# Kernel tuning notes

Measured on AMD Instinct MI355X. Metric: run time of the kernel, lower is better.

Reference implementation:

```python
import jax, jax.numpy as jnp
import numpy as np

N, E = 50000, 800000
C_IN, C_HID, C_OUT = 64, 128, 64
BN_EPS = 1e-5


def setup_inputs() -> dict:
    key = jax.random.key(0)
    ks = jax.random.split(key, 8)
    s1 = 1.0 / np.sqrt(C_IN)
    s2 = 1.0 / np.sqrt(C_HID)
    return {
        "x": jax.random.normal(ks[0], (N, C_IN), dtype=jnp.float32),
        "edge_index": jax.random.randint(ks[1], (2, E), 0, N, dtype=jnp.int64),
        # message MLP: in -> hidden -> out
        "W1": jax.random.uniform(ks[2], (C_IN, C_HID), jnp.float32, -s1, s1),
        "b1": jnp.zeros((C_HID,), jnp.float32),
        "W2": jax.random.uniform(ks[3], (C_HID, C_OUT), jnp.float32, -s2, s2),
        "b2": jnp.zeros((C_OUT,), jnp.float32),
        # root/self transform
        "W_root": jax.random.uniform(ks[4], (C_IN, C_OUT), jnp.float32, -s1, s1),
        "b_root": jnp.zeros((C_OUT,), jnp.float32),
        # PReLU (single shared parameter, torch default 0.25)
        "prelu_w": jnp.full((1,), 0.25, jnp.float32),
        # BatchNorm affine params
        "bn_gamma": jnp.ones((C_OUT,), jnp.float32),
        "bn_beta": jnp.zeros((C_OUT,), jnp.float32),
    }


def reference(x, edge_index, W1, b1, W2, b2, W_root, b_root, prelu_w, bn_gamma, bn_beta):
    src, dst = edge_index[0], edge_index[1]
    # gather -> per-edge message MLP: [E, C_hid] -> [E, C_out]
    m = jax.nn.relu(x[src] @ W1 + b1) @ W2 + b2
    # scatter-sum to destination nodes: [N, C_out]
    agg = jax.ops.segment_sum(m, dst, num_segments=N)
    h = agg + x @ W_root + b_root
    # PReLU
    h = jnp.where(h >= 0, h, prelu_w * h)
    # BatchNorm over nodes (training-mode batch stats, biased var)
    mu = jnp.mean(h, axis=0)
    var = jnp.mean(jnp.square(h - mu), axis=0)
    h = (h - mu) * jax.lax.rsqrt(var + BN_EPS) * bn_gamma + bn_beta
    return h
```

## Files before the change

### kernel.cpp

```cpp
#include <hip/hip_runtime.h>

#define NNODES 50000
#define NEDGES 800000
#define NTILES 3125
#define CAP    64

typedef __attribute__((ext_vector_type(8))) short bf16x8;
typedef __attribute__((ext_vector_type(4))) float f32x4;

union FragU { uint u[4]; bf16x8 v; };

__device__ __forceinline__ uint bfr(float f) {
    uint u = __float_as_uint(f);
    return (u + 0x7fffu + ((u >> 16) & 1u)) >> 16;
}
__device__ __forceinline__ uint pack_bf2(float a, float b) {
    return bfr(a) | (bfr(b) << 16);
}
__device__ __forceinline__ float bf2f(uint hi16) {
    return __uint_as_float(hi16 << 16);
}

__global__ __launch_bounds__(256) void mlp_root_kernel(
    const float* __restrict__ x,
    const float* __restrict__ W1, const float* __restrict__ b1,
    const float* __restrict__ W2, const float* __restrict__ b2,
    const float* __restrict__ Wr, const float* __restrict__ br,
    ushort* __restrict__ M16, float* __restrict__ R)
{
    __shared__ uint  sFrag[40 * 256];
    __shared__ float sb1[128];
    __shared__ float sb2[64];
    __shared__ float sbr[64];
    __shared__ uint  sH[4 * 16 * 68];

    const int tid = threadIdx.x;
    for (int idx = tid; idx < 40 * 256; idx += 256) {
        const int f  = idx >> 8;
        const int ln = (idx >> 2) & 63;
        const int d  = idx & 3;
        const int g = ln >> 4, r = ln & 15;
        const int j0 = 2 * d;
        float w0, w1v;
        if (f < 16) {
            const int mt = f >> 1, ks = f & 1;
            const int k = 32 * ks + 8 * g + j0, c = 16 * mt + r;
            w0 = W1[k * 128 + c];  w1v = W1[(k + 1) * 128 + c];
        } else if (f < 32) {
            const int mt = (f - 16) >> 2, ks = (f - 16) & 3;
            const int k = 32 * ks + 8 * g + j0, c = 16 * mt + r;
            w0 = W2[k * 64 + c];   w1v = W2[(k + 1) * 64 + c];
        } else {
            const int mt = (f - 32) >> 1, ks = (f - 32) & 1;
            const int k = 32 * ks + 8 * g + j0, c = 16 * mt + r;
            w0 = Wr[k * 64 + c];   w1v = Wr[(k + 1) * 64 + c];
        }
        sFrag[idx] = pack_bf2(w0, w1v);
    }
    if (tid < 128) sb1[tid] = b1[tid];
    if (tid < 64)  { sb2[tid] = b2[tid]; sbr[tid] = br[tid]; }
    __syncthreads();

    const int lane = tid & 63;
    const int g = lane >> 4, r = lane & 15;
    uint* Hw = &sH[(tid >> 6) * 16 * 68];
    uint* Mu = (uint*)M16;
    const int gw  = blockIdx.x * 4 + (tid >> 6);
    const int nwv = gridDim.x * 4;

#define LOADFRAG(f) (*(const bf16x8*)&sFrag[((f) << 8) | (lane << 2)])

    for (int t = gw; t < NTILES; t += nwv) {
        const int node = t * 16 + r;
        bf16x8 xf[2];
#pragma unroll
        for (int ks = 0; ks < 2; ++ks) {
            const float4 f0 = *(const float4*)&x[node * 64 + 32 * ks + 8 * g];
            const float4 f1 = *(const float4*)&x[node * 64 + 32 * ks + 8 * g + 4];
            FragU fx;
            fx.u[0] = pack_bf2(f0.x, f0.y); fx.u[1] = pack_bf2(f0.z, f0.w);
            fx.u[2] = pack_bf2(f1.x, f1.y); fx.u[3] = pack_bf2(f1.z, f1.w);
            xf[ks] = fx.v;
        }
#pragma unroll
        for (int mt = 0; mt < 8; ++mt) {
            f32x4 a = {0.f, 0.f, 0.f, 0.f};
            a = __builtin_amdgcn_mfma_f32_16x16x32_bf16(LOADFRAG(2 * mt), xf[0], a, 0, 0, 0);
            a = __builtin_amdgcn_mfma_f32_16x16x32_bf16(LOADFRAG(2 * mt + 1), xf[1], a, 0, 0, 0);
            const int hc = 16 * mt + 4 * g;
            const float v0 = fmaxf(a[0] + sb1[hc + 0], 0.f);
            const float v1 = fmaxf(a[1] + sb1[hc + 1], 0.f);
            const float v2 = fmaxf(a[2] + sb1[hc + 2], 0.f);
            const float v3 = fmaxf(a[3] + sb1[hc + 3], 0.f);
            const int hd = r * 68 + 8 * mt + 2 * g;
            Hw[hd]     = pack_bf2(v0, v1);
            Hw[hd + 1] = pack_bf2(v2, v3);
        }
        bf16x8 hf[4];
#pragma unroll
        for (int ks = 0; ks < 4; ++ks)
            hf[ks] = *(const bf16x8*)&Hw[r * 68 + 16 * ks + 4 * g];
#pragma unroll
        for (int mt = 0; mt < 4; ++mt) {
            f32x4 a2 = {0.f, 0.f, 0.f, 0.f};
#pragma unroll
            for (int ks = 0; ks < 4; ++ks)
                a2 = __builtin_amdgcn_mfma_f32_16x16x32_bf16(LOADFRAG(16 + 4 * mt + ks), hf[ks], a2, 0, 0, 0);
            f32x4 ar = {0.f, 0.f, 0.f, 0.f};
            ar = __builtin_amdgcn_mfma_f32_16x16x32_bf16(LOADFRAG(32 + 2 * mt), xf[0], ar, 0, 0, 0);
            ar = __builtin_amdgcn_mfma_f32_16x16x32_bf16(LOADFRAG(32 + 2 * mt + 1), xf[1], ar, 0, 0, 0);
            const int oc = 16 * mt + 4 * g;
            const float m0 = a2[0] + sb2[oc + 0], m1 = a2[1] + sb2[oc + 1];
            const float m2 = a2[2] + sb2[oc + 2], m3 = a2[3] + sb2[oc + 3];
            uint2 mp = make_uint2(pack_bf2(m0, m1), pack_bf2(m2, m3));
            *(uint2*)&Mu[node * 32 + 8 * mt + 2 * g] = mp;
            float4 rv = make_float4(ar[0] + sbr[oc + 0], ar[1] + sbr[oc + 1],
                                    ar[2] + sbr[oc + 2], ar[3] + sbr[oc + 3]);
            *(float4*)&R[node * 64 + oc] = rv;
        }
    }
#undef LOADFRAG
}

__global__ __launch_bounds__(256) void fill_kernel(
    const int* __restrict__ ei, int* __restrict__ cnt, int* __restrict__ bucket)
{
    const int e = blockIdx.x * 256 + threadIdx.x;
    const int dst = ei[NEDGES + e];
    const int pos = atomicAdd(&cnt[dst], 1);
    if (pos < CAP) bucket[dst * CAP + pos] = ei[e];
}

__global__ __launch_bounds__(256) void gather_prelu_stats_kernel(
    const int* __restrict__ cnt, const int* __restrict__ bucket,
    const ushort* __restrict__ M16, const float* __restrict__ pw,
    float* __restrict__ h, float* __restrict__ stats)
{
    __shared__ float ls[128];
    const int tid = threadIdx.x;
    if (tid < 128) ls[tid] = 0.f;
    __syncthreads();

    const int lane = tid & 63;
    const int gw   = (blockIdx.x * 256 + tid) >> 6;
    const int nwv  = (gridDim.x * 256) >> 6;
    const float p  = pw[0];
    float sum = 0.f, sumsq = 0.f;

    for (int n = gw; n < NNODES; n += nwv) {
        int c = cnt[n]; c = c > CAP ? CAP : c;
        const int sall = bucket[n * CAP + lane];
        float a0 = 0.f, a1 = 0.f, a2 = 0.f, a3 = 0.f;
        int i = 0;
        for (; i + 4 <= c; i += 4) {
            const int s0 = __shfl(sall, i),     s1 = __shfl(sall, i + 1);
            const int s2 = __shfl(sall, i + 2), s3 = __shfl(sall, i + 3);
            a0 += bf2f(M16[s0 * 64 + lane]);
            a1 += bf2f(M16[s1 * 64 + lane]);
            a2 += bf2f(M16[s2 * 64 + lane]);
            a3 += bf2f(M16[s3 * 64 + lane]);
        }
        for (; i < c; ++i) a0 += bf2f(M16[__shfl(sall, i) * 64 + lane]);
        float v = h[n * 64 + lane] + ((a0 + a1) + (a2 + a3));
        v = (v >= 0.f) ? v : p * v;
        h[n * 64 + lane] = v;
        sum += v;
        sumsq = fmaf(v, v, sumsq);
    }
    atomicAdd(&ls[lane], sum);
    atomicAdd(&ls[64 + lane], sumsq);
    __syncthreads();
    if (tid < 128) atomicAdd(&stats[tid], ls[tid]);
}

__global__ __launch_bounds__(256) void bn_kernel(
    float* __restrict__ h, const float* __restrict__ stats,
    const float* __restrict__ gamma, const float* __restrict__ beta)
{
    const int lane  = threadIdx.x & 63;
    const float inv = 1.0f / (float)NNODES;
    const float mu  = stats[lane] * inv;
    const float var = stats[64 + lane] * inv - mu * mu;
    const float rs  = rsqrtf(var + 1e-5f);
    const float gsc = gamma[lane] * rs;
    const float bt  = beta[lane];
    const int total  = NNODES * 64;
    const int stride = gridDim.x * 256;
    for (int i = blockIdx.x * 256 + threadIdx.x; i < total; i += stride)
        h[i] = (h[i] - mu) * gsc + bt;
}

extern "C" void kernel_launch(void* const* d_in, const int* in_sizes, int n_in,
                              void* d_out, int out_size, void* d_ws, size_t ws_size,
                              hipStream_t stream) {
    const float* x     = (const float*)d_in[0];
    const int*   ei    = (const int*)d_in[1];
    const float* W1    = (const float*)d_in[2];
    const float* b1    = (const float*)d_in[3];
    const float* W2    = (const float*)d_in[4];
    const float* b2    = (const float*)d_in[5];
    const float* Wr    = (const float*)d_in[6];
    const float* br    = (const float*)d_in[7];
    const float* pw    = (const float*)d_in[8];
    const float* gamma = (const float*)d_in[9];
    const float* beta  = (const float*)d_in[10];

    float* out = (float*)d_out;

    char* ws = (char*)d_ws;
    ushort* M16   = (ushort*)ws;
    int*    bucket= (int*)(ws + 6400000);
    int*    cnt   = (int*)(ws + 6400000 + 12800000);
    float*  stats = (float*)(ws + 6400000 + 12800000 + 200000);

    hipMemsetAsync(cnt, 0, 200000 + 512, stream);

    mlp_root_kernel<<<512, 256, 0, stream>>>(x, W1, b1, W2, b2, Wr, br, M16, out);
    fill_kernel<<<NEDGES / 256, 256, 0, stream>>>(ei, cnt, bucket);
    gather_prelu_stats_kernel<<<2048, 256, 0, stream>>>(cnt, bucket, M16, pw, out, stats);
    bn_kernel<<<2048, 256, 0, stream>>>(out, stats, gamma, beta);
}
```

Baseline: 228.5 us.

## Compact edge buckets to 16-bit, widen gather loads, precompute weight table, vectorize BN

Weight fragments and biases are packed once by a small prep kernel into a global table, which each MLP block copies into LDS with vector loads. Edge buckets store 16-bit source ids, halving bucket traffic; this relies on the node count fitting in 16 bits. The gather kernel reads 32-bit words (two bf16 values) per lane, with the two half-waves handling different edges and 16 edges per iteration, then combines the halves with shuffles. BatchNorm is rewritten as one float4 per thread with no loop.

Result: faster. 215.5 us (-5.7%).

```diff
diff --git a/kernel.cpp b/kernel.cpp
--- a/kernel.cpp
+++ b/kernel.cpp
@@ -21,26 +21,18 @@
     return __uint_as_float(hi16 << 16);
 }
 
-__global__ __launch_bounds__(256) void mlp_root_kernel(
-    const float* __restrict__ x,
+__global__ __launch_bounds__(256) void prep_kernel(
     const float* __restrict__ W1, const float* __restrict__ b1,
     const float* __restrict__ W2, const float* __restrict__ b2,
     const float* __restrict__ Wr, const float* __restrict__ br,
-    ushort* __restrict__ M16, float* __restrict__ R)
-{
-    __shared__ uint  sFrag[40 * 256];
-    __shared__ float sb1[128];
-    __shared__ float sb2[64];
-    __shared__ float sbr[64];
-    __shared__ uint  sH[4 * 16 * 68];
-
+    uint* __restrict__ tbl)
+{
+    const int f = blockIdx.x;
     const int tid = threadIdx.x;
-    for (int idx = tid; idx < 40 * 256; idx += 256) {
-        const int f  = idx >> 8;
-        const int ln = (idx >> 2) & 63;
-        const int d  = idx & 3;
+    if (f < 40) {
+        const int ln = tid >> 2, dd = tid & 3;
         const int g = ln >> 4, r = ln & 15;
-        const int j0 = 2 * d;
+        const int j0 = 2 * dd;
         float w0, w1v;
         if (f < 16) {
             const int mt = f >> 1, ks = f & 1;
@@ -55,11 +47,34 @@
             const int k = 32 * ks + 8 * g + j0, c = 16 * mt + r;
             w0 = Wr[k * 64 + c];   w1v = Wr[(k + 1) * 64 + c];
         }
-        sFrag[idx] = pack_bf2(w0, w1v);
-    }
-    if (tid < 128) sb1[tid] = b1[tid];
-    if (tid < 64)  { sb2[tid] = b2[tid]; sbr[tid] = br[tid]; }
+        tbl[f * 256 + tid] = pack_bf2(w0, w1v);
+    } else {
+        if (tid < 128) tbl[10240 + tid] = __float_as_uint(b1[tid]);
+        if (tid < 64) {
+            tbl[10368 + tid] = __float_as_uint(b2[tid]);
+            tbl[10432 + tid] = __float_as_uint(br[tid]);
+        }
+    }
+}
+
+__global__ __launch_bounds__(256) void mlp_root_kernel(
+    const float* __restrict__ x, const uint* __restrict__ tbl,
+    ushort* __restrict__ M16, float* __restrict__ R)
+{
+    __shared__ uint sTab[10496];
+    __shared__ uint sH[4 * 16 * 68];
+
+    const int tid = threadIdx.x;
+    {
+        uint4* s4 = (uint4*)sTab;
+        const uint4* t4 = (const uint4*)tbl;
+        for (int i = tid; i < 2624; i += 256) s4[i] = t4[i];
+    }
     __syncthreads();
+    const uint*  sFrag = sTab;
+    const float* sb1 = (const float*)&sTab[10240];
+    const float* sb2 = (const float*)&sTab[10368];
+    const float* sbr = (const float*)&sTab[10432];
 
     const int lane = tid & 63;
     const int g = lane >> 4, r = lane & 15;
@@ -123,17 +138,17 @@
 }
 
 __global__ __launch_bounds__(256) void fill_kernel(
-    const int* __restrict__ ei, int* __restrict__ cnt, int* __restrict__ bucket)
+    const int* __restrict__ ei, int* __restrict__ cnt, ushort* __restrict__ bucketU)
 {
     const int e = blockIdx.x * 256 + threadIdx.x;
     const int dst = ei[NEDGES + e];
     const int pos = atomicAdd(&cnt[dst], 1);
-    if (pos < CAP) bucket[dst * CAP + pos] = ei[e];
+    if (pos < CAP) bucketU[dst * CAP + pos] = (ushort)ei[e];
 }
 
 __global__ __launch_bounds__(256) void gather_prelu_stats_kernel(
-    const int* __restrict__ cnt, const int* __restrict__ bucket,
-    const ushort* __restrict__ M16, const float* __restrict__ pw,
+    const int* __restrict__ cnt, const ushort* __restrict__ bucketU,
+    const uint* __restrict__ M32, const float* __restrict__ pw,
     float* __restrict__ h, float* __restrict__ stats)
 {
     __shared__ float ls[128];
@@ -142,6 +157,8 @@
     __syncthreads();
 
     const int lane = tid & 63;
+    const int half = lane >> 5;
+    const int dw   = lane & 31;
     const int gw   = (blockIdx.x * 256 + tid) >> 6;
     const int nwv  = (gridDim.x * 256) >> 6;
     const float p  = pw[0];
@@ -149,19 +166,37 @@
 
     for (int n = gw; n < NNODES; n += nwv) {
         int c = cnt[n]; c = c > CAP ? CAP : c;
-        const int sall = bucket[n * CAP + lane];
-        float a0 = 0.f, a1 = 0.f, a2 = 0.f, a3 = 0.f;
+        const int   sv = (int)bucketU[n * CAP + lane];
+        const float hv = h[n * 64 + lane];
+        float aL0 = 0.f, aL1 = 0.f, aH0 = 0.f, aH1 = 0.f;
         int i = 0;
-        for (; i + 4 <= c; i += 4) {
-            const int s0 = __shfl(sall, i),     s1 = __shfl(sall, i + 1);
-            const int s2 = __shfl(sall, i + 2), s3 = __shfl(sall, i + 3);
-            a0 += bf2f(M16[s0 * 64 + lane]);
-            a1 += bf2f(M16[s1 * 64 + lane]);
-            a2 += bf2f(M16[s2 * 64 + lane]);
-            a3 += bf2f(M16[s3 * 64 + lane]);
-        }
-        for (; i < c; ++i) a0 += bf2f(M16[__shfl(sall, i) * 64 + lane]);
-        float v = h[n * 64 + lane] + ((a0 + a1) + (a2 + a3));
+        for (; i + 16 <= c; i += 16) {
+#pragma unroll
+            for (int j = 0; j < 8; ++j) {
+                const int s = __shfl(sv, i + 2 * j + half);
+                const uint mv = M32[s * 32 + dw];
+                if (j & 1) { aL1 += bf2f(mv & 0xffffu); aH1 += bf2f(mv >> 16); }
+                else       { aL0 += bf2f(mv & 0xffffu); aH0 += bf2f(mv >> 16); }
+            }
+        }
+        if (i < c) {
+#pragma unroll
+            for (int j = 0; j < 8; ++j) {
+                const int idx = i + 2 * j + half;
+                const int s = __shfl(sv, idx & 63);
+                if (idx < c) {
+                    const uint mv = M32[s * 32 + dw];
+                    if (j & 1) { aL1 += bf2f(mv & 0xffffu); aH1 += bf2f(mv >> 16); }
+                    else       { aL0 += bf2f(mv & 0xffffu); aH0 += bf2f(mv >> 16); }
+                }
+            }
+        }
+        float aL = aL0 + aL1, aH = aH0 + aH1;
+        aL += __shfl_xor(aL, 32);
+        aH += __shfl_xor(aH, 32);
+        const float vlo = __shfl(aL, lane >> 1);
+        const float vhi = __shfl(aH, lane >> 1);
+        float v = hv + ((lane & 1) ? vhi : vlo);
         v = (v >= 0.f) ? v : p * v;
         h[n * 64 + lane] = v;
         sum += v;
@@ -174,20 +209,23 @@
 }
 
 __global__ __launch_bounds__(256) void bn_kernel(
-    float* __restrict__ h, const float* __restrict__ stats,
+    float4* __restrict__ h, const float* __restrict__ stats,
     const float* __restrict__ gamma, const float* __restrict__ beta)
 {
-    const int lane  = threadIdx.x & 63;
+    const int i  = blockIdx.x * 256 + threadIdx.x;
+    const int c0 = (i & 15) * 4;
     const float inv = 1.0f / (float)NNODES;
-    const float mu  = stats[lane] * inv;
-    const float var = stats[64 + lane] * inv - mu * mu;
-    const float rs  = rsqrtf(var + 1e-5f);
-    const float gsc = gamma[lane] * rs;
-    const float bt  = beta[lane];
-    const int total  = NNODES * 64;
-    const int stride = gridDim.x * 256;
-    for (int i = blockIdx.x * 256 + threadIdx.x; i < total; i += stride)
-        h[i] = (h[i] - mu) * gsc + bt;
+    const float4 s1 = *(const float4*)&stats[c0];
+    const float4 s2 = *(const float4*)&stats[64 + c0];
+    const float4 gm = *(const float4*)&gamma[c0];
+    const float4 bt = *(const float4*)&beta[c0];
+    float4 v = h[i];
+    float mu, var;
+    mu = s1.x * inv; var = s2.x * inv - mu * mu; v.x = (v.x - mu) * (gm.x * rsqrtf(var + 1e-5f)) + bt.x;
+    mu = s1.y * inv; var = s2.y * inv - mu * mu; v.y = (v.y - mu) * (gm.y * rsqrtf(var + 1e-5f)) + bt.y;
+    mu = s1.z * inv; var = s2.z * inv - mu * mu; v.z = (v.z - mu) * (gm.z * rsqrtf(var + 1e-5f)) + bt.z;
+    mu = s1.w * inv; var = s2.w * inv - mu * mu; v.w = (v.w - mu) * (gm.w * rsqrtf(var + 1e-5f)) + bt.w;
+    h[i] = v;
 }
 
 extern "C" void kernel_launch(void* const* d_in, const int* in_sizes, int n_in,
@@ -208,15 +246,17 @@
     float* out = (float*)d_out;
 
     char* ws = (char*)d_ws;
-    ushort* M16   = (ushort*)ws;
-    int*    bucket= (int*)(ws + 6400000);
-    int*    cnt   = (int*)(ws + 6400000 + 12800000);
-    float*  stats = (float*)(ws + 6400000 + 12800000 + 200000);
+    ushort* M16    = (ushort*)ws;
+    ushort* bucketU= (ushort*)(ws + 6400000);
+    int*    cnt    = (int*)(ws + 12800000);
+    float*  stats  = (float*)(ws + 12800000 + 200000);
+    uint*   tbl    = (uint*)(ws + 12800000 + 200000 + 512);
 
     hipMemsetAsync(cnt, 0, 200000 + 512, stream);
 
-    mlp_root_kernel<<<512, 256, 0, stream>>>(x, W1, b1, W2, b2, Wr, br, M16, out);
-    fill_kernel<<<NEDGES / 256, 256, 0, stream>>>(ei, cnt, bucket);
-    gather_prelu_stats_kernel<<<2048, 256, 0, stream>>>(cnt, bucket, M16, pw, out, stats);
-    bn_kernel<<<2048, 256, 0, stream>>>(out, stats, gamma, beta);
-}
+    prep_kernel<<<41, 256, 0, stream>>>(W1, b1, W2, b2, Wr, br, tbl);
+    fill_kernel<<<NEDGES / 256, 256, 0, stream>>>(ei, cnt, bucketU);
+    mlp_root_kernel<<<512, 256, 0, stream>>>(x, tbl, M16, out);
+    gather_prelu_stats_kernel<<<2048, 256, 0, stream>>>(cnt, bucketU, (const uint*)M16, pw, out, stats);
+    bn_kernel<<<3125, 256, 0, stream>>>((float4*)out, stats, gamma, beta);
+}
```
